# Performance work log

Hardware: AMD Instinct MI355X
Metric: run time of the kernel (lower is better)

Reference implementation:

```python
import jax, jax.numpy as jnp
import numpy as np

NUM_HEADS = 16
LN_EPS = 1e-05


def setup_inputs() -> dict:
    key = jax.random.key(0)
    ks = jax.random.split(key, 10)
    B, S, H = 2, 2048, 1024
    s = 1.0 / np.sqrt(H)
    return {
        "hidden_states": jax.random.normal(ks[0], (B, S, H), dtype=jnp.float32),
        "Wq": jax.random.normal(ks[1], (H, H), dtype=jnp.float32) * s,
        "bq": jax.random.normal(ks[2], (H,), dtype=jnp.float32) * 0.02,
        "Wk": jax.random.normal(ks[3], (H, H), dtype=jnp.float32) * s,
        "bk": jax.random.normal(ks[4], (H,), dtype=jnp.float32) * 0.02,
        "Wv": jax.random.normal(ks[5], (H, H), dtype=jnp.float32) * s,
        "bv": jax.random.normal(ks[6], (H,), dtype=jnp.float32) * 0.02,
        "Wd": jax.random.normal(ks[7], (H, H), dtype=jnp.float32) * s,
        "bd": jax.random.normal(ks[8], (H,), dtype=jnp.float32) * 0.02,
        "ln_gamma": jnp.ones((H,), dtype=jnp.float32),
        "ln_beta": jnp.zeros((H,), dtype=jnp.float32),
    }


def reference(hidden_states, Wq, bq, Wk, bk, Wv, bv, Wd, bd, ln_gamma, ln_beta):
    B, S, H = hidden_states.shape
    nh = NUM_HEADS
    hd = H // nh

    # QKV projections (torch Linear: x @ W.T + b), split heads -> [B, nh, S, hd]
    def proj(W, b):
        y = jnp.einsum('bsh,oh->bso', hidden_states, W) + b
        return y.reshape(B, S, nh, hd).transpose(0, 2, 1, 3)

    q = proj(Wq, bq)
    k = proj(Wk, bk)
    v = proj(Wv, bv)

    # scaled dot-product attention: [B, nh, S, S]
    scores = jnp.einsum('bhqd,bhkd->bhqk', q, k) / jnp.sqrt(jnp.float32(hd))
    probs = jax.nn.softmax(scores, axis=-1)
    ctx = jnp.einsum('bhqk,bhkd->bhqd', probs, v)  # [B, nh, S, hd]
    ctx = ctx.transpose(0, 2, 1, 3).reshape(B, S, H)

    # output dense + residual + LayerNorm
    attn_out = jnp.einsum('bsh,oh->bso', ctx, Wd) + bd
    x = attn_out + hidden_states
    mu = jnp.mean(x, axis=-1, keepdims=True)
    var = jnp.mean(jnp.square(x - mu), axis=-1, keepdims=True)
    return (x - mu) * jax.lax.rsqrt(var + LN_EPS) * ln_gamma + ln_beta
```

## Files before the change

### kernel.cpp

```cpp
#include <hip/hip_runtime.h>

constexpr int kH    = 1024;
constexpr int kSEQ  = 2048;
constexpr int kBATCH= 2;
constexpr int kNH   = 16;
constexpr int kHD   = 64;
constexpr int kM    = 4096;

typedef _Float16 h8  __attribute__((ext_vector_type(8)));
typedef _Float16 h4  __attribute__((ext_vector_type(4)));
typedef float   f32x4 __attribute__((ext_vector_type(4)));

static __device__ __forceinline__ f32x4 mfma16(h8 a, h8 b, f32x4 c) {
  return __builtin_amdgcn_mfma_f32_16x16x32_f16(a, b, c, 0, 0, 0);
}

static __device__ __forceinline__ void gll16(const _Float16* g, _Float16* l) {
  __builtin_amdgcn_global_load_lds(
      (const __attribute__((address_space(1))) void*)g,
      (__attribute__((address_space(3))) void*)l, 16, 0, 0);
}

#define QSCALE 0.18033688011112042f
#define C0INIT (-5.770780163555854f)

__global__ __launch_bounds__(256) void cvt_all(
    const float* __restrict__ X,  const float* __restrict__ Wq,
    const float* __restrict__ Wk, const float* __restrict__ Wv,
    const float* __restrict__ Wd,
    _Float16* __restrict__ Xh,  _Float16* __restrict__ Wqh,
    _Float16* __restrict__ Wkh, _Float16* __restrict__ Wvh,
    _Float16* __restrict__ Wdh)
{
  int i = blockIdx.x * 256 + threadIdx.x;
  const float* src; _Float16* dst; int off;
  if (i < (kM * kH) / 4) {
    src = X; dst = Xh; off = i;
  } else {
    int j = i - (kM * kH) / 4;
    int w = j >> 18;
    off = j & 262143;
    src = (w == 0) ? Wq : (w == 1) ? Wk : (w == 2) ? Wv : Wd;
    dst = (w == 0) ? Wqh : (w == 1) ? Wkh : (w == 2) ? Wvh : Wdh;
  }
  float4 v = reinterpret_cast<const float4*>(src)[off];
  h4 o;
  o[0] = (_Float16)v.x; o[1] = (_Float16)v.y;
  o[2] = (_Float16)v.z; o[3] = (_Float16)v.w;
  reinterpret_cast<h4*>(dst)[off] = o;
}

__global__ __launch_bounds__(256, 3) void qkv_gemm(
    const _Float16* __restrict__ Xh,
    const _Float16* __restrict__ Wq, const _Float16* __restrict__ Wk,
    const _Float16* __restrict__ Wv,
    const float* __restrict__ bq, const float* __restrict__ bk,
    const float* __restrict__ bv,
    _Float16* __restrict__ Qo, _Float16* __restrict__ Ko, _Float16* __restrict__ Vo)
{
  const int proj = blockIdx.z;
  const _Float16* W   = (proj == 0) ? Wq : ((proj == 1) ? Wk : Wv);
  const float*    bias= (proj == 0) ? bq : ((proj == 1) ? bk : bv);
  _Float16*       Out = (proj == 0) ? Qo : ((proj == 1) ? Ko : Vo);

  const int m0 = blockIdx.y * 128, n0 = blockIdx.x * 128;
  __shared__ __align__(16) char qsmem[32768];
  _Float16* const As = (_Float16*)qsmem;
  _Float16* const Bs = (_Float16*)(qsmem + 16384);
  _Float16* const Lt = (_Float16*)qsmem;

  const int tid  = threadIdx.x;
  const int wave = tid >> 6, lane = tid & 63, quad = lane >> 4, l16 = lane & 15;
  const int mw = (wave & 1) * 64, nw = (wave >> 1) * 64;

  f32x4 acc[4][4] = {};
  const int grow = wave * 32 + (lane >> 2);
  const int gcol = (lane & 3) * 8;
  const _Float16* Ag = Xh + (size_t)(m0 + grow) * kH + gcol;
  const _Float16* Bg = W  + (size_t)(n0 + grow) * kH + gcol;

  {
    gll16(Ag,            &As[wave * 1024]);
    gll16(Ag + 16 * kH,  &As[wave * 1024 + 512]);
    gll16(Bg,            &Bs[wave * 1024]);
    gll16(Bg + 16 * kH,  &Bs[wave * 1024 + 512]);
  }

  for (int k = 0; k < 32; ++k) {
    const int cur = k & 1;
    __syncthreads();
    if (k < 31) {
      const int k0 = (k + 1) * 32, nb = cur ^ 1;
      gll16(Ag + k0,           &As[nb * 4096 + wave * 1024]);
      gll16(Ag + 16 * kH + k0, &As[nb * 4096 + wave * 1024 + 512]);
      gll16(Bg + k0,           &Bs[nb * 4096 + wave * 1024]);
      gll16(Bg + 16 * kH + k0, &Bs[nb * 4096 + wave * 1024 + 512]);
    }
    h8 af[4], bf[4];
    #pragma unroll
    for (int mi = 0; mi < 4; ++mi)
      af[mi] = *reinterpret_cast<const h8*>(&As[cur * 4096 + (mw + mi * 16 + l16) * 32 + quad * 8]);
    #pragma unroll
    for (int ni = 0; ni < 4; ++ni)
      bf[ni] = *reinterpret_cast<const h8*>(&Bs[cur * 4096 + (nw + ni * 16 + l16) * 32 + quad * 8]);
    #pragma unroll
    for (int mi = 0; mi < 4; ++mi)
      #pragma unroll
      for (int ni = 0; ni < 4; ++ni)
        acc[mi][ni] = mfma16(af[mi], bf[ni], acc[mi][ni]);
  }

  if (proj != 2) {
    #pragma unroll
    for (int mi = 0; mi < 4; ++mi)
    #pragma unroll
    for (int ni = 0; ni < 4; ++ni) {
      const int ng = n0 + nw + ni * 16 + l16;
      const float bv_ = bias[ng];
      const int hh = ng >> 6, dd = ng & 63;
      #pragma unroll
      for (int r = 0; r < 4; ++r) {
        const int mg = m0 + mw + mi * 16 + quad * 4 + r;
        float val = acc[mi][ni][r] + bv_;
        if (proj == 0) val *= QSCALE;
        const int bb = mg >> 11, srow = mg & 2047;
        Out[(((size_t)(bb * kNH + hh) * kSEQ) + srow) * kHD + dd] = (_Float16)val;
      }
    }
  } else {
    __syncthreads();
    #pragma unroll
    for (int mi = 0; mi < 4; ++mi)
    #pragma unroll
    for (int ni = 0; ni < 4; ++ni) {
      const int ng = n0 + nw + ni * 16 + l16;
      const float bv_ = bias[ng];
      const int nl = nw + ni * 16 + l16;
      const int c16 = (mw >> 3) + mi * 2 + (quad >> 1);
      const int cs = c16 ^ (nl & 15);
      h4 pp;
      pp[0] = (_Float16)(acc[mi][ni][0] + bv_);
      pp[1] = (_Float16)(acc[mi][ni][1] + bv_);
      pp[2] = (_Float16)(acc[mi][ni][2] + bv_);
      pp[3] = (_Float16)(acc[mi][ni][3] + bv_);
      *reinterpret_cast<h4*>(&Lt[nl * 128 + cs * 8 + (quad & 1) * 4]) = pp;
    }
    __syncthreads();
    const int bb = m0 >> 11, srow0 = m0 & 2047;
    const int nl2 = tid >> 1, half = tid & 1;
    const int ng2 = n0 + nl2, hh2 = ng2 >> 6, dd2 = ng2 & 63;
    _Float16* dst = Out + ((size_t)(bb * kNH + hh2) * kHD + dd2) * kSEQ
                        + srow0 + half * 64;
    const int hperm = dd2 & 15;
    const int hx = hperm >> 1;
    const bool hswap = (hperm & 1);
    #pragma unroll
    for (int j = 0; j < 8; ++j) {
      const int c = half * 8 + j;
      const int cs = c ^ (nl2 & 15);
      h8 v = *reinterpret_cast<const h8*>(&Lt[nl2 * 128 + cs * 8]);
      if (hswap) {
        h8 vs;
        vs[0] = v[4]; vs[1] = v[5]; vs[2] = v[6]; vs[3] = v[7];
        vs[4] = v[0]; vs[5] = v[1]; vs[6] = v[2]; vs[7] = v[3];
        v = vs;
      }
      *reinterpret_cast<h8*>(dst + (j ^ hx) * 8) = v;
    }
  }
}

__global__ __launch_bounds__(512, 4) void attn_kernel(
    const _Float16* __restrict__ Q, const _Float16* __restrict__ K,
    const _Float16* __restrict__ Vt, _Float16* __restrict__ Ctx)
{
  const int qt = blockIdx.x, bh = blockIdx.y;
  const int tid = threadIdx.x;
  const int wave = tid >> 6, lane = tid & 63, quad = lane >> 4, l16 = lane & 15;
  const int sw = l16 & 7;
  const int qw = wave & 3;
  const int wg = wave >> 2;

  __shared__ __align__(16) char smem[35328];
  _Float16* const Kl = (_Float16*)smem;
  _Float16* const Vl = (_Float16*)(smem + 16384);
  float* const Ored = (float*)smem;
  float* const Lred = (float*)(smem + 34816);

  const _Float16* Qb = Q  + (size_t)bh * kSEQ * kHD;
  const _Float16* Kb = K  + (size_t)bh * kSEQ * kHD;
  const _Float16* Vb = Vt + (size_t)bh * kHD * kSEQ;

  const int qbase = qt * 128 + qw * 32;
  h8 qf[2][2];
  #pragma unroll
  for (int qh = 0; qh < 2; ++qh)
    #pragma unroll
    for (int dh = 0; dh < 2; ++dh)
      qf[qh][dh] = *reinterpret_cast<const h8*>(
          &Qb[(size_t)(qbase + qh * 16 + l16) * kHD + dh * 32 + quad * 8]);

  const int srow0  = lane >> 3;
  const int schunk = (lane & 7) ^ srow0;
  const int krow   = wave * 8 + srow0;
  const _Float16* Kg = Kb + (size_t)krow * kHD + schunk * 8;
  const _Float16* Vg = Vb + (size_t)krow * kSEQ + (lane & 7) * 8;

  const int slotA = 8 * wg + quad;
  const int offA = ((slotA    ) ^ l16) << 2;
  const int offB = ((slotA + 4) ^ l16) << 2;

  float l_acc[2] = {0.f, 0.f};
  f32x4 o[2][4] = {};

  gll16(Kg, &Kl[(wave * 8) * 64]);
  gll16(Vg, &Vl[(wave * 8) * 64]);

  for (int kt = 0; kt < kSEQ / 64; ++kt) {
    const int cur = kt & 1;
    __syncthreads();
    if (kt + 1 < kSEQ / 64) {
      const int nb = cur ^ 1;
      const size_t ko = (size_t)(kt + 1) * 64;
      gll16(Kg + ko * kHD, &Kl[nb * 4096 + (wave * 8) * 64]);
      gll16(Vg + ko,       &Vl[nb * 4096 + (wave * 8) * 64]);
    }
    const _Float16* Kc = Kl + cur * 4096;
    const _Float16* Vc = Vl + cur * 4096;

    h8 ka[2][2];
    #pragma unroll
    for (int nt = 0; nt < 2; ++nt) {
      const int keyl = wg * 32 + nt * 16 + l16;
      ka[nt][0] = *reinterpret_cast<const h8*>(&Kc[keyl * 64 + ((quad    ) ^ sw) * 8]);
      ka[nt][1] = *reinterpret_cast<const h8*>(&Kc[keyl * 64 + ((quad ^ 4) ^ sw) * 8]);
    }
    f32x4 s[2][2];
    __builtin_amdgcn_s_setprio(1);
    #pragma unroll
    for (int nt = 0; nt < 2; ++nt)
      #pragma unroll
      for (int qh = 0; qh < 2; ++qh) {
        f32x4 a = {C0INIT, C0INIT, C0INIT, C0INIT};
        a = mfma16(ka[nt][0], qf[qh][0], a);
        a = mfma16(ka[nt][1], qf[qh][1], a);
        s[nt][qh] = a;
      }
    __builtin_amdgcn_s_setprio(0);

    h8 pa[2];
    #pragma unroll
    for (int qh = 0; qh < 2; ++qh) {
      float e00 = __builtin_amdgcn_exp2f(s[0][qh][0]);
      float e01 = __builtin_amdgcn_exp2f(s[0][qh][1]);
      float e02 = __builtin_amdgcn_exp2f(s[0][qh][2]);
      float e03 = __builtin_amdgcn_exp2f(s[0][qh][3]);
      float e10 = __builtin_amdgcn_exp2f(s[1][qh][0]);
      float e11 = __builtin_amdgcn_exp2f(s[1][qh][1]);
      float e12 = __builtin_amdgcn_exp2f(s[1][qh][2]);
      float e13 = __builtin_amdgcn_exp2f(s[1][qh][3]);
      l_acc[qh] += ((e00 + e01) + (e02 + e03)) + ((e10 + e11) + (e12 + e13));
      h8 p;
      p[0] = (_Float16)e00; p[1] = (_Float16)e01;
      p[2] = (_Float16)e02; p[3] = (_Float16)e03;
      p[4] = (_Float16)e10; p[5] = (_Float16)e11;
      p[6] = (_Float16)e12; p[7] = (_Float16)e13;
      pa[qh] = p;
    }

    __builtin_amdgcn_s_setprio(1);
    #pragma unroll
    for (int dt = 0; dt < 4; ++dt) {
      const _Float16* vr = &Vc[(dt * 16 + l16) * 64];
      h4 va  = *reinterpret_cast<const h4*>(vr + offA);
      h4 vbb = *reinterpret_cast<const h4*>(vr + offB);
      h8 v8;
      v8[0] = va[0];  v8[1] = va[1];  v8[2] = va[2];  v8[3] = va[3];
      v8[4] = vbb[0]; v8[5] = vbb[1]; v8[6] = vbb[2]; v8[7] = vbb[3];
      o[0][dt] = mfma16(pa[0], v8, o[0][dt]);
      o[1][dt] = mfma16(pa[1], v8, o[1][dt]);
    }
    __builtin_amdgcn_s_setprio(0);
  }

  float li[2] = {l_acc[0], l_acc[1]};
  #pragma unroll
  for (int qh = 0; qh < 2; ++qh) {
    li[qh] += __shfl_xor(li[qh], 16);
    li[qh] += __shfl_xor(li[qh], 32);
  }

  __syncthreads();
  if (wg == 1) {
    float* myO = Ored + (qw * 64 + lane) * 34;
    #pragma unroll
    for (int qh = 0; qh < 2; ++qh)
      #pragma unroll
      for (int dt = 0; dt < 4; ++dt) {
        reinterpret_cast<float2*>(&myO[qh * 16 + dt * 4])[0] =
            reinterpret_cast<const float2*>(&o[qh][dt])[0];
        reinterpret_cast<float2*>(&myO[qh * 16 + dt * 4 + 2])[0] =
            reinterpret_cast<const float2*>(&o[qh][dt])[1];
      }
    if (quad == 0) {
      Lred[(qw * 2 + 0) * 16 + l16] = li[0];
      Lred[(qw * 2 + 1) * 16 + l16] = li[1];
    }
  }
  __syncthreads();
  if (wg == 1) return;

  const float* pO = Ored + (qw * 64 + lane) * 34;
  #pragma unroll
  for (int qh = 0; qh < 2; ++qh) {
    #pragma unroll
    for (int dt = 0; dt < 4; ++dt) {
      float2 a = reinterpret_cast<const float2*>(&pO[qh * 16 + dt * 4])[0];
      float2 b2 = reinterpret_cast<const float2*>(&pO[qh * 16 + dt * 4 + 2])[0];
      o[qh][dt][0] += a.x;  o[qh][dt][1] += a.y;
      o[qh][dt][2] += b2.x; o[qh][dt][3] += b2.y;
    }
    li[qh] = 1.f / (li[qh] + Lred[(qw * 2 + qh) * 16 + l16]);
  }
  const int b = bh >> 4, hh = bh & 15;
  #pragma unroll
  for (int qh = 0; qh < 2; ++qh)
    #pragma unroll
    for (int r = 0; r < 4; ++r) {
      const float linv = __shfl(li[qh], quad * 4 + r);
      const int srow = qbase + qh * 16 + quad * 4 + r;
      #pragma unroll
      for (int dt = 0; dt < 4; ++dt) {
        const int col = hh * kHD + dt * 16 + l16;
        Ctx[((size_t)(b * kSEQ + srow)) * kH + col] = (_Float16)(o[qh][dt][r] * linv);
      }
    }
}

__global__ __launch_bounds__(256, 2) void dense_gemm(
    const _Float16* __restrict__ A, const _Float16* __restrict__ W,
    const float* __restrict__ bias, const float* __restrict__ resid,
    float* __restrict__ Out)
{
  const int m0 = blockIdx.y * 128, n0 = blockIdx.x * 64;
  __shared__ __align__(16) _Float16 As[2][128 * 32];
  __shared__ __align__(16) _Float16 Bs[2][64 * 32];
  const int tid  = threadIdx.x;
  const int wave = tid >> 6, lane = tid & 63, quad = lane >> 4, l16 = lane & 15;
  const int mw = (wave & 1) * 64, nw = (wave >> 1) * 32;
  f32x4 acc[4][2] = {};
  const int growA = wave * 32 + (lane >> 2);
  const int growB = wave * 16 + (lane >> 2);
  const int gcol = (lane & 3) * 8;
  const _Float16* Ag = A + (size_t)(m0 + growA) * kH + gcol;
  const _Float16* Bg = W + (size_t)(n0 + growB) * kH + gcol;

  {
    gll16(Ag,           &As[0][wave * 1024]);
    gll16(Ag + 16 * kH, &As[0][wave * 1024 + 512]);
    gll16(Bg,           &Bs[0][wave * 512]);
  }

  for (int k = 0; k < 32; ++k) {
    const int cur = k & 1;
    __syncthreads();
    if (k < 31) {
      const int k0 = (k + 1) * 32, nb = cur ^ 1;
      gll16(Ag + k0,           &As[nb][wave * 1024]);
      gll16(Ag + 16 * kH + k0, &As[nb][wave * 1024 + 512]);
      gll16(Bg + k0,           &Bs[nb][wave * 512]);
    }
    h8 af[4], bf[2];
    #pragma unroll
    for (int mi = 0; mi < 4; ++mi)
      af[mi] = *reinterpret_cast<const h8*>(&As[cur][(mw + mi * 16 + l16) * 32 + quad * 8]);
    #pragma unroll
    for (int ni = 0; ni < 2; ++ni)
      bf[ni] = *reinterpret_cast<const h8*>(&Bs[cur][(nw + ni * 16 + l16) * 32 + quad * 8]);
    #pragma unroll
    for (int mi = 0; mi < 4; ++mi)
      #pragma unroll
      for (int ni = 0; ni < 2; ++ni)
        acc[mi][ni] = mfma16(af[mi], bf[ni], acc[mi][ni]);
  }
  #pragma unroll
  for (int mi = 0; mi < 4; ++mi)
  #pragma unroll
  for (int ni = 0; ni < 2; ++ni) {
    const int ng = n0 + nw + ni * 16 + l16;
    const float bv_ = bias[ng];
    #pragma unroll
    for (int r = 0; r < 4; ++r) {
      const int mg = m0 + mw + mi * 16 + quad * 4 + r;
      Out[(size_t)mg * kH + ng] = acc[mi][ni][r] + bv_ + resid[(size_t)mg * kH + ng];
    }
  }
}

__global__ __launch_bounds__(256) void ln_kernel(const float* __restrict__ Tmp,
    const float* __restrict__ gamma, const float* __restrict__ beta,
    float* __restrict__ out)
{
  const int row = blockIdx.x;
  const float4 v = reinterpret_cast<const float4*>(Tmp + (size_t)row * kH)[threadIdx.x];
  float s  = v.x + v.y + v.z + v.w;
  float ss = v.x * v.x + v.y * v.y + v.z * v.z + v.w * v.w;
  #pragma unroll
  for (int off = 32; off > 0; off >>= 1) {
    s  += __shfl_down(s, off);
    ss += __shfl_down(ss, off);
  }
  __shared__ float red[8];
  const int wave = threadIdx.x >> 6, lane = threadIdx.x & 63;
  if (lane == 0) { red[wave] = s; red[4 + wave] = ss; }
  __syncthreads();
  s  = red[0] + red[1] + red[2] + red[3];
  ss = red[4] + red[5] + red[6] + red[7];
  const float mu   = s * (1.f / kH);
  const float var  = ss * (1.f / kH) - mu * mu;
  const float rstd = rsqrtf(var + 1e-5f);
  const float4 g  = reinterpret_cast<const float4*>(gamma)[threadIdx.x];
  const float4 bb = reinterpret_cast<const float4*>(beta)[threadIdx.x];
  float4 o;
  o.x = (v.x - mu) * rstd * g.x + bb.x;
  o.y = (v.y - mu) * rstd * g.y + bb.y;
  o.z = (v.z - mu) * rstd * g.z + bb.z;
  o.w = (v.w - mu) * rstd * g.w + bb.w;
  reinterpret_cast<float4*>(out + (size_t)row * kH)[threadIdx.x] = o;
}

extern "C" void kernel_launch(void* const* d_in, const int* in_sizes, int n_in,
                              void* d_out, int out_size, void* d_ws, size_t ws_size,
                              hipStream_t stream) {
  const float* hs    = (const float*)d_in[0];
  const float* Wq    = (const float*)d_in[1];
  const float* bq    = (const float*)d_in[2];
  const float* Wk    = (const float*)d_in[3];
  const float* bk    = (const float*)d_in[4];
  const float* Wv    = (const float*)d_in[5];
  const float* bv    = (const float*)d_in[6];
  const float* Wd    = (const float*)d_in[7];
  const float* bd    = (const float*)d_in[8];
  const float* gamma = (const float*)d_in[9];
  const float* beta  = (const float*)d_in[10];
  float* out = (float*)d_out;

  char* ws = (char*)d_ws;
  _Float16* Xh  = (_Float16*)(ws + 0);
  _Float16* Wqh = (_Float16*)(ws + 8388608);
  _Float16* Wkh = (_Float16*)(ws + 10485760);
  _Float16* Wvh = (_Float16*)(ws + 12582912);
  _Float16* Wdh = (_Float16*)(ws + 14680064);
  _Float16* Qh  = (_Float16*)(ws + 16777216);
  _Float16* Kh  = (_Float16*)(ws + 25165824);
  _Float16* Vth = (_Float16*)(ws + 33554432);
  _Float16* Ch  = (_Float16*)(ws + 41943040);
  float*    Tmp = (float*)Qh;

  cvt_all<<<8192, 256, 0, stream>>>(hs, Wq, Wk, Wv, Wd, Xh, Wqh, Wkh, Wvh, Wdh);
  qkv_gemm<<<dim3(kH / 128, kM / 128, 3), 256, 0, stream>>>(
      Xh, Wqh, Wkh, Wvh, bq, bk, bv, Qh, Kh, Vth);
  attn_kernel<<<dim3(kSEQ / 128, kBATCH * kNH), 512, 0, stream>>>(Qh, Kh, Vth, Ch);
  dense_gemm<<<dim3(kH / 64, kM / 128), 256, 0, stream>>>(Ch, Wdh, bd, hs, Tmp);
  ln_kernel<<<kM, 256, 0, stream>>>(Tmp, gamma, beta, out);
}
```

Baseline: 201.3 us.

## Triple-buffer K/V tiles in attention with explicit vmcnt waits

Replaces double buffering of K/V tiles in LDS with a three-stage ring buffer, issuing loads two tiles ahead. Each tile waits only on its own loads via s_waitcnt vmcnt(2) and a raw s_barrier, instead of a full __syncthreads that drains every outstanding load. The goal is to hide global-to-LDS latency behind the MFMA work. In exchange LDS per block grows from about 35KB to 48KB, which may reduce how many blocks fit on a CU. The V fragment assembly also changes to a shufflevector.

```diff
diff --git a/kernel.cpp b/kernel.cpp
--- a/kernel.cpp
+++ b/kernel.cpp
@@ -181,9 +181,9 @@
   const int qw = wave & 3;
   const int wg = wave >> 2;
 
-  __shared__ __align__(16) char smem[35328];
+  __shared__ __align__(16) char smem[49152];
   _Float16* const Kl = (_Float16*)smem;
-  _Float16* const Vl = (_Float16*)(smem + 16384);
+  _Float16* const Vl = (_Float16*)(smem + 24576);
   float* const Ored = (float*)smem;
   float* const Lred = (float*)(smem + 34816);
 
@@ -213,21 +213,13 @@
   float l_acc[2] = {0.f, 0.f};
   f32x4 o[2][4] = {};
 
-  gll16(Kg, &Kl[(wave * 8) * 64]);
-  gll16(Vg, &Vl[(wave * 8) * 64]);
-
-  for (int kt = 0; kt < kSEQ / 64; ++kt) {
-    const int cur = kt & 1;
-    __syncthreads();
-    if (kt + 1 < kSEQ / 64) {
-      const int nb = cur ^ 1;
-      const size_t ko = (size_t)(kt + 1) * 64;
-      gll16(Kg + ko * kHD, &Kl[nb * 4096 + (wave * 8) * 64]);
-      gll16(Vg + ko,       &Vl[nb * 4096 + (wave * 8) * 64]);
-    }
-    const _Float16* Kc = Kl + cur * 4096;
-    const _Float16* Vc = Vl + cur * 4096;
-
+  auto STAGE = [&](int kt2, int buf) {
+    const size_t ko = (size_t)kt2 * 64;
+    gll16(Kg + ko * kHD, &Kl[buf * 4096 + (wave * 8) * 64]);
+    gll16(Vg + ko,       &Vl[buf * 4096 + (wave * 8) * 64]);
+  };
+
+  auto COMPUTE = [&](const _Float16* Kc, const _Float16* Vc) {
     h8 ka[2][2];
     #pragma unroll
     for (int nt = 0; nt < 2; ++nt) {
@@ -274,14 +266,38 @@
       const _Float16* vr = &Vc[(dt * 16 + l16) * 64];
       h4 va  = *reinterpret_cast<const h4*>(vr + offA);
       h4 vbb = *reinterpret_cast<const h4*>(vr + offB);
-      h8 v8;
-      v8[0] = va[0];  v8[1] = va[1];  v8[2] = va[2];  v8[3] = va[3];
-      v8[4] = vbb[0]; v8[5] = vbb[1]; v8[6] = vbb[2]; v8[7] = vbb[3];
+      h8 v8 = __builtin_shufflevector(va, vbb, 0, 1, 2, 3, 4, 5, 6, 7);
       o[0][dt] = mfma16(pa[0], v8, o[0][dt]);
       o[1][dt] = mfma16(pa[1], v8, o[1][dt]);
     }
     __builtin_amdgcn_s_setprio(0);
-  }
+  };
+
+  STAGE(0, 0);
+  STAGE(1, 1);
+
+  int cur = 0;
+  for (int kt = 0; kt < 30; ++kt) {
+    asm volatile("s_waitcnt vmcnt(2)" ::: "memory");
+    __builtin_amdgcn_sched_barrier(0);
+    __builtin_amdgcn_s_barrier();
+    __builtin_amdgcn_sched_barrier(0);
+    int nb = cur + 2; if (nb >= 3) nb -= 3;
+    STAGE(kt + 2, nb);
+    COMPUTE(Kl + cur * 4096, Vl + cur * 4096);
+    cur = (cur + 1 == 3) ? 0 : cur + 1;
+  }
+  asm volatile("s_waitcnt vmcnt(2)" ::: "memory");
+  __builtin_amdgcn_sched_barrier(0);
+  __builtin_amdgcn_s_barrier();
+  __builtin_amdgcn_sched_barrier(0);
+  COMPUTE(Kl + cur * 4096, Vl + cur * 4096);
+  cur = (cur + 1 == 3) ? 0 : cur + 1;
+  asm volatile("s_waitcnt vmcnt(0)" ::: "memory");
+  __builtin_amdgcn_sched_barrier(0);
+  __builtin_amdgcn_s_barrier();
+  __builtin_amdgcn_sched_barrier(0);
+  COMPUTE(Kl + cur * 4096, Vl + cur * 4096);
 
   float li[2] = {l_acc[0], l_acc[1]};
   #pragma unroll
```

New measurement: 202.2 us. About the same (+0.5%).
